# Optimization experiments

Measured on AMD Instinct MI355X. Metric: run time of the kernel, lower is better.

Reference implementation:

```python
import jax, jax.numpy as jnp
import numpy as np

B, S, H = 32, 4096, 512

def setup_inputs() -> dict:
    key = jax.random.key(0)
    k1, k2, k3 = jax.random.split(key, 3)
    h_t = jax.random.normal(k1, (B, H), dtype=jnp.float32)
    context = jax.random.normal(k2, (B, S, H), dtype=jnp.float32)
    W = jax.random.normal(k3, (H, H), dtype=jnp.float32) * (1.0 / np.sqrt(H))
    pos = 7  # current cyclic-buffer write index (self.it % seq_len)
    return {"h_t": h_t, "context": context, "W": W, "pos": pos}

def reference(h_t, context, W, pos):
    # Luong 'general' attention: score[b,s] = h_t[b] . (W @ context[b,s])
    scores = jnp.einsum('bh,hk,bsk->bs', h_t, W, context)  # [B,S]
    attn = jax.nn.softmax(scores, axis=-1)                  # softmax over buffer slots
    # weighted sum over the context buffer -> [B,H]
    cntx = jnp.einsum('bs,bsh->bh', attn, context)
    # cyclic buffer write: add_vector(h_t) at slot pos (detached in original)
    new_buffer = context.at[:, pos % context.shape[1], :].set(h_t)
    return cntx, new_buffer
```

## Files before the change

kernel.cpp:

```cpp
#include <hip/hip_runtime.h>
#include <math.h>

constexpr int B = 32, S = 4096, H = 512;
constexpr int BDIM = 256;
constexpr int MAX_SPLIT = 64;
constexpr float LOG2E = 1.44269504088896340736f;
constexpr float DEFER_THR = 11.5415603f;

typedef float f4 __attribute__((ext_vector_type(4)));

__global__ __launch_bounds__(BDIM) void u_kernel(const float* __restrict__ h_t,
                                                 const float* __restrict__ W,
                                                 float* __restrict__ u) {
    const int b = blockIdx.y;
    const int k = blockIdx.x * BDIM + threadIdx.x;
    __shared__ float hs[H];
    for (int i = threadIdx.x; i < H; i += BDIM) hs[i] = h_t[b * H + i];
    __syncthreads();
    float a0 = 0.f, a1 = 0.f, a2 = 0.f, a3 = 0.f;
#pragma unroll 8
    for (int h = 0; h < H; h += 4) {
        a0 = fmaf(hs[h],     W[(size_t)(h)     * H + k], a0);
        a1 = fmaf(hs[h + 1], W[(size_t)(h + 1) * H + k], a1);
        a2 = fmaf(hs[h + 2], W[(size_t)(h + 2) * H + k], a2);
        a3 = fmaf(hs[h + 3], W[(size_t)(h + 3) * H + k], a3);
    }
    u[b * H + k] = ((a0 + a1) + (a2 + a3)) * LOG2E;
}

__global__ __launch_bounds__(BDIM) void flash_kernel(const float* __restrict__ ctx,
                                                     const float* __restrict__ h_t,
                                                     const float* __restrict__ u,
                                                     const int* __restrict__ posp,
                                                     float* __restrict__ newbuf,
                                                     float* __restrict__ pacc,
                                                     float* __restrict__ pml,
                                                     int nsplit) {
    const int b     = blockIdx.y;
    const int split = blockIdx.x;
    const int w     = threadIdx.x >> 6;
    const int lane  = threadIdx.x & 63;
    const int rpb   = S / nsplit;
    const int s0    = split * rpb;
    int pos = posp[0] % S; if (pos < 0) pos += S;

    const f4* ub = (const f4*)(u + (size_t)b * H);
    const f4 u0 = ub[lane], u1 = ub[64 + lane];
    const f4* hb = (const f4*)(h_t + (size_t)b * H);
    const f4 h0 = hb[lane], h1 = hb[64 + lane];

    float m = -INFINITY, l = 0.f;
    f4 a0 = {0.f, 0.f, 0.f, 0.f}, a1 = {0.f, 0.f, 0.f, 0.f};

#pragma unroll 4
    for (int s = s0 + w; s < s0 + rpb; s += 4) {
        const f4* crow = (const f4*)(ctx + ((size_t)b * S + s) * H);
        const f4 c0 = crow[lane];
        const f4 c1 = crow[64 + lane];

        f4* orow = (f4*)(newbuf + ((size_t)b * S + s) * H);
        const f4 o0 = (s == pos) ? h0 : c0;
        const f4 o1 = (s == pos) ? h1 : c1;
        __builtin_nontemporal_store(o0, orow + lane);
        __builtin_nontemporal_store(o1, orow + 64 + lane);

        float d = c0.x * u0.x + c0.y * u0.y + c0.z * u0.z + c0.w * u0.w
                + c1.x * u1.x + c1.y * u1.y + c1.z * u1.z + c1.w * u1.w;
#pragma unroll
        for (int off = 32; off >= 1; off >>= 1) d += __shfl_xor(d, off);

        if (d > m + DEFER_THR) {
            const float sc = exp2f(m - d);
            a0 *= sc; a1 *= sc; l *= sc; m = d;
        }
        const float p = exp2f(d - m);
        a0 += p * c0;
        a1 += p * c1;
        l  += p;
    }

    __shared__ float lacc[4][H];
    __shared__ float lml[4][2];
    f4* dst = (f4*)&lacc[w][0];
    dst[lane] = a0; dst[64 + lane] = a1;
    if (lane == 0) { lml[w][0] = m; lml[w][1] = l; }
    __syncthreads();

    const float m0 = lml[0][0], m1 = lml[1][0], m2 = lml[2][0], m3 = lml[3][0];
    const float M  = fmaxf(fmaxf(m0, m1), fmaxf(m2, m3));
    const float e0 = exp2f(m0 - M), e1 = exp2f(m1 - M);
    const float e2 = exp2f(m2 - M), e3 = exp2f(m3 - M);

    const int t    = threadIdx.x;
    const int pidx = b * nsplit + split;
    const float ca = e0 * lacc[0][t]       + e1 * lacc[1][t]
                   + e2 * lacc[2][t]       + e3 * lacc[3][t];
    const float cb = e0 * lacc[0][256 + t] + e1 * lacc[1][256 + t]
                   + e2 * lacc[2][256 + t] + e3 * lacc[3][256 + t];
    pacc[(size_t)pidx * H + t]       = ca;
    pacc[(size_t)pidx * H + 256 + t] = cb;
    if (t == 0) {
        const float L = e0 * lml[0][1] + e1 * lml[1][1]
                      + e2 * lml[2][1] + e3 * lml[3][1];
        pml[2 * pidx] = M; pml[2 * pidx + 1] = L;
    }
}

__global__ __launch_bounds__(BDIM) void combine_kernel(const float* __restrict__ pacc,
                                                       const float* __restrict__ pml,
                                                       float* __restrict__ cntx,
                                                       int nsplit) {
    const int b    = blockIdx.x;
    const int half = blockIdx.y;
    const int t    = threadIdx.x;
    const int col  = half * 256 + t;

    __shared__ float lm[MAX_SPLIT], ll[MAX_SPLIT];
    for (int p = t; p < nsplit; p += BDIM) {
        lm[p] = pml[2 * (b * nsplit + p)];
        ll[p] = pml[2 * (b * nsplit + p) + 1];
    }
    __syncthreads();

    float M = -INFINITY;
    for (int p = 0; p < nsplit; ++p) M = fmaxf(M, lm[p]);

    float acc = 0.f, L = 0.f;
#pragma unroll 4
    for (int p = 0; p < nsplit; ++p) {
        const float e = exp2f(lm[p] - M);
        L   = fmaf(e, ll[p], L);
        acc = fmaf(e, pacc[(size_t)(b * nsplit + p) * H + col], acc);
    }
    cntx[b * H + col] = acc / L;
}

extern "C" void kernel_launch(void* const* d_in, const int* in_sizes, int n_in,
                              void* d_out, int out_size, void* d_ws, size_t ws_size,
                              hipStream_t stream) {
    const float* h_t = (const float*)d_in[0];
    const float* ctx = (const float*)d_in[1];
    const float* W   = (const float*)d_in[2];
    const int*   pos = (const int*)d_in[3];

    float* out    = (float*)d_out;
    float* cntx   = out;
    float* newbuf = out + (size_t)B * H;

    char*  ws = (char*)d_ws;
    float* u  = (float*)ws;
    const size_t u_bytes = (size_t)B * H * sizeof(float);

    int nsplit = MAX_SPLIT;
    while (nsplit > 1) {
        const size_t need = u_bytes
                          + (size_t)B * nsplit * H * sizeof(float)
                          + (size_t)B * nsplit * 2 * sizeof(float);
        if (need <= ws_size) break;
        nsplit >>= 1;
    }
    float* pacc = (float*)(ws + u_bytes);
    float* pml  = pacc + (size_t)B * nsplit * H;

    u_kernel<<<dim3(H / BDIM, B), BDIM, 0, stream>>>(h_t, W, u);
    flash_kernel<<<dim3(nsplit, B), BDIM, 0, stream>>>(ctx, h_t, u, pos, newbuf,
                                                       pacc, pml, nsplit);
    combine_kernel<<<dim3(B, 2), BDIM, 0, stream>>>(pacc, pml, cntx, nsplit);
}
```

Baseline: 122.6 us.

## Software-pipeline context loads with two independent softmax streams per warp

Measured after the change: 119.0 us, median of 2. 1.03x faster.

```diff
diff --git a/kernel.cpp b/kernel.cpp
--- a/kernel.cpp
+++ b/kernel.cpp
@@ -8,6 +8,15 @@
 constexpr float DEFER_THR = 11.5415603f;
 
 typedef float f4 __attribute__((ext_vector_type(4)));
+
+__device__ __forceinline__ float dot8(const f4 c0, const f4 c1,
+                                      const f4 u0, const f4 u1) {
+    float d = c0.x * u0.x;
+    d = fmaf(c0.y, u0.y, d); d = fmaf(c0.z, u0.z, d); d = fmaf(c0.w, u0.w, d);
+    d = fmaf(c1.x, u1.x, d); d = fmaf(c1.y, u1.y, d);
+    d = fmaf(c1.z, u1.z, d); d = fmaf(c1.w, u1.w, d);
+    return d;
+}
 
 __global__ __launch_bounds__(BDIM) void u_kernel(const float* __restrict__ h_t,
                                                  const float* __restrict__ W,
@@ -29,9 +38,7 @@
 }
 
 __global__ __launch_bounds__(BDIM) void flash_kernel(const float* __restrict__ ctx,
-                                                     const float* __restrict__ h_t,
                                                      const float* __restrict__ u,
-                                                     const int* __restrict__ posp,
                                                      float* __restrict__ newbuf,
                                                      float* __restrict__ pacc,
                                                      float* __restrict__ pml,
@@ -42,78 +49,114 @@
     const int lane  = threadIdx.x & 63;
     const int rpb   = S / nsplit;
     const int s0    = split * rpb;
-    int pos = posp[0] % S; if (pos < 0) pos += S;
+    const int halfr = rpb >> 1;
 
     const f4* ub = (const f4*)(u + (size_t)b * H);
     const f4 u0 = ub[lane], u1 = ub[64 + lane];
-    const f4* hb = (const f4*)(h_t + (size_t)b * H);
-    const f4 h0 = hb[lane], h1 = hb[64 + lane];
-
-    float m = -INFINITY, l = 0.f;
-    f4 a0 = {0.f, 0.f, 0.f, 0.f}, a1 = {0.f, 0.f, 0.f, 0.f};
-
-#pragma unroll 4
-    for (int s = s0 + w; s < s0 + rpb; s += 4) {
-        const f4* crow = (const f4*)(ctx + ((size_t)b * S + s) * H);
-        const f4 c0 = crow[lane];
-        const f4 c1 = crow[64 + lane];
-
-        f4* orow = (f4*)(newbuf + ((size_t)b * S + s) * H);
-        const f4 o0 = (s == pos) ? h0 : c0;
-        const f4 o1 = (s == pos) ? h1 : c1;
-        __builtin_nontemporal_store(o0, orow + lane);
-        __builtin_nontemporal_store(o1, orow + 64 + lane);
-
-        float d = c0.x * u0.x + c0.y * u0.y + c0.z * u0.z + c0.w * u0.w
-                + c1.x * u1.x + c1.y * u1.y + c1.z * u1.z + c1.w * u1.w;
-#pragma unroll
-        for (int off = 32; off >= 1; off >>= 1) d += __shfl_xor(d, off);
-
-        if (d > m + DEFER_THR) {
-            const float sc = exp2f(m - d);
-            a0 *= sc; a1 *= sc; l *= sc; m = d;
+
+    const size_t baseA = (size_t)b * S + s0;
+    const size_t baseB = baseA + halfr;
+
+    float mA = -INFINITY, lA = 0.f; f4 aA0 = {0,0,0,0}, aA1 = {0,0,0,0};
+    float mB = -INFINITY, lB = 0.f; f4 aB0 = {0,0,0,0}, aB1 = {0,0,0,0};
+
+    int r = w;
+    const f4* pA = (const f4*)(ctx + (baseA + r) * H);
+    const f4* pB = (const f4*)(ctx + (baseB + r) * H);
+    f4 cA0 = pA[lane], cA1 = pA[64 + lane];
+    f4 cB0 = pB[lane], cB1 = pB[64 + lane];
+
+    while (r < halfr) {
+        const int rn = r + 4;
+        const int rs = (rn < halfr) ? rn : r;
+        const f4* nA = (const f4*)(ctx + (baseA + rs) * H);
+        const f4* nB = (const f4*)(ctx + (baseB + rs) * H);
+        const f4 nA0 = nA[lane], nA1 = nA[64 + lane];
+        const f4 nB0 = nB[lane], nB1 = nB[64 + lane];
+
+        f4* oA = (f4*)(newbuf + (baseA + r) * H);
+        f4* oB = (f4*)(newbuf + (baseB + r) * H);
+        __builtin_nontemporal_store(cA0, oA + lane);
+        __builtin_nontemporal_store(cA1, oA + 64 + lane);
+        __builtin_nontemporal_store(cB0, oB + lane);
+        __builtin_nontemporal_store(cB1, oB + 64 + lane);
+
+        float dA = dot8(cA0, cA1, u0, u1);
+        float dB = dot8(cB0, cB1, u0, u1);
+#pragma unroll
+        for (int off = 32; off >= 1; off >>= 1) {
+            dA += __shfl_xor(dA, off);
+            dB += __shfl_xor(dB, off);
         }
-        const float p = exp2f(d - m);
-        a0 += p * c0;
-        a1 += p * c1;
-        l  += p;
-    }
-
-    __shared__ float lacc[4][H];
-    __shared__ float lml[4][2];
-    f4* dst = (f4*)&lacc[w][0];
-    dst[lane] = a0; dst[64 + lane] = a1;
-    if (lane == 0) { lml[w][0] = m; lml[w][1] = l; }
+
+        if (dA > mA + DEFER_THR) {
+            const float sc = exp2f(mA - dA);
+            aA0 *= sc; aA1 *= sc; lA *= sc; mA = dA;
+        }
+        if (dB > mB + DEFER_THR) {
+            const float sc = exp2f(mB - dB);
+            aB0 *= sc; aB1 *= sc; lB *= sc; mB = dB;
+        }
+        const float pAe = exp2f(dA - mA);
+        const float pBe = exp2f(dB - mB);
+        aA0 += pAe * cA0; aA1 += pAe * cA1; lA += pAe;
+        aB0 += pBe * cB0; aB1 += pBe * cB1; lB += pBe;
+
+        cA0 = nA0; cA1 = nA1; cB0 = nB0; cB1 = nB1;
+        r = rn;
+    }
+
+    __shared__ float lacc[8][H];
+    __shared__ float lml[8][2];
+    f4* dA_ = (f4*)&lacc[w][0];
+    f4* dB_ = (f4*)&lacc[4 + w][0];
+    dA_[lane] = aA0; dA_[64 + lane] = aA1;
+    dB_[lane] = aB0; dB_[64 + lane] = aB1;
+    if (lane == 0) {
+        lml[w][0] = mA;     lml[w][1] = lA;
+        lml[4 + w][0] = mB; lml[4 + w][1] = lB;
+    }
     __syncthreads();
 
-    const float m0 = lml[0][0], m1 = lml[1][0], m2 = lml[2][0], m3 = lml[3][0];
-    const float M  = fmaxf(fmaxf(m0, m1), fmaxf(m2, m3));
-    const float e0 = exp2f(m0 - M), e1 = exp2f(m1 - M);
-    const float e2 = exp2f(m2 - M), e3 = exp2f(m3 - M);
+    float M = -INFINITY;
+#pragma unroll
+    for (int j = 0; j < 8; ++j) M = fmaxf(M, lml[j][0]);
+    float e[8];
+#pragma unroll
+    for (int j = 0; j < 8; ++j) e[j] = exp2f(lml[j][0] - M);
 
     const int t    = threadIdx.x;
     const int pidx = b * nsplit + split;
-    const float ca = e0 * lacc[0][t]       + e1 * lacc[1][t]
-                   + e2 * lacc[2][t]       + e3 * lacc[3][t];
-    const float cb = e0 * lacc[0][256 + t] + e1 * lacc[1][256 + t]
-                   + e2 * lacc[2][256 + t] + e3 * lacc[3][256 + t];
+    float ca = 0.f, cb = 0.f;
+#pragma unroll
+    for (int j = 0; j < 8; ++j) {
+        ca = fmaf(e[j], lacc[j][t], ca);
+        cb = fmaf(e[j], lacc[j][256 + t], cb);
+    }
     pacc[(size_t)pidx * H + t]       = ca;
     pacc[(size_t)pidx * H + 256 + t] = cb;
     if (t == 0) {
-        const float L = e0 * lml[0][1] + e1 * lml[1][1]
-                      + e2 * lml[2][1] + e3 * lml[3][1];
+        float L = 0.f;
+#pragma unroll
+        for (int j = 0; j < 8; ++j) L = fmaf(e[j], lml[j][1], L);
         pml[2 * pidx] = M; pml[2 * pidx + 1] = L;
     }
 }
 
 __global__ __launch_bounds__(BDIM) void combine_kernel(const float* __restrict__ pacc,
                                                        const float* __restrict__ pml,
+                                                       const float* __restrict__ h_t,
+                                                       const int* __restrict__ posp,
+                                                       float* __restrict__ newbuf,
                                                        float* __restrict__ cntx,
                                                        int nsplit) {
     const int b    = blockIdx.x;
     const int half = blockIdx.y;
     const int t    = threadIdx.x;
     const int col  = half * 256 + t;
+
+    int pos = posp[0] % S; if (pos < 0) pos += S;
+    newbuf[((size_t)b * S + pos) * H + col] = h_t[b * H + col];
 
     __shared__ float lm[MAX_SPLIT], ll[MAX_SPLIT];
     for (int p = t; p < nsplit; p += BDIM) {
@@ -163,7 +206,8 @@
     float* pml  = pacc + (size_t)B * nsplit * H;
 
     u_kernel<<<dim3(H / BDIM, B), BDIM, 0, stream>>>(h_t, W, u);
-    flash_kernel<<<dim3(nsplit, B), BDIM, 0, stream>>>(ctx, h_t, u, pos, newbuf,
+    flash_kernel<<<dim3(nsplit, B), BDIM, 0, stream>>>(ctx, u, newbuf,
                                                        pacc, pml, nsplit);
-    combine_kernel<<<dim3(B, 2), BDIM, 0, stream>>>(pacc, pml, cntx, nsplit);
-}
+    combine_kernel<<<dim3(B, 2), BDIM, 0, stream>>>(pacc, pml, h_t, pos,
+                                                    newbuf, cntx, nsplit);
+}
```

## Process two rows per wavefront, split rows contiguously, move pos write to combine

Applied to the files above, without the earlier changes.

Result: no change. 122.2 us (-0.3%).

```diff
diff --git a/kernel.cpp b/kernel.cpp
--- a/kernel.cpp
+++ b/kernel.cpp
@@ -3,7 +3,7 @@
 
 constexpr int B = 32, S = 4096, H = 512;
 constexpr int BDIM = 256;
-constexpr int MAX_SPLIT = 64;
+constexpr int MAX_SPLIT = 128;
 constexpr float LOG2E = 1.44269504088896340736f;
 constexpr float DEFER_THR = 11.5415603f;
 
@@ -29,9 +29,7 @@
 }
 
 __global__ __launch_bounds__(BDIM) void flash_kernel(const float* __restrict__ ctx,
-                                                     const float* __restrict__ h_t,
                                                      const float* __restrict__ u,
-                                                     const int* __restrict__ posp,
                                                      float* __restrict__ newbuf,
                                                      float* __restrict__ pacc,
                                                      float* __restrict__ pml,
@@ -40,56 +38,86 @@
     const int split = blockIdx.x;
     const int w     = threadIdx.x >> 6;
     const int lane  = threadIdx.x & 63;
+    const int g     = lane >> 5;
+    const int j     = lane & 31;
     const int rpb   = S / nsplit;
-    const int s0    = split * rpb;
-    int pos = posp[0] % S; if (pos < 0) pos += S;
+    const int rpw   = rpb / 4;
+    const int s0    = split * rpb + w * rpw;
 
     const f4* ub = (const f4*)(u + (size_t)b * H);
-    const f4 u0 = ub[lane], u1 = ub[64 + lane];
-    const f4* hb = (const f4*)(h_t + (size_t)b * H);
-    const f4 h0 = hb[lane], h1 = hb[64 + lane];
+    f4 uf[4];
+#pragma unroll
+    for (int k = 0; k < 4; ++k) uf[k] = ub[j + 32 * k];
 
     float m = -INFINITY, l = 0.f;
-    f4 a0 = {0.f, 0.f, 0.f, 0.f}, a1 = {0.f, 0.f, 0.f, 0.f};
-
-#pragma unroll 4
-    for (int s = s0 + w; s < s0 + rpb; s += 4) {
-        const f4* crow = (const f4*)(ctx + ((size_t)b * S + s) * H);
-        const f4 c0 = crow[lane];
-        const f4 c1 = crow[64 + lane];
-
-        f4* orow = (f4*)(newbuf + ((size_t)b * S + s) * H);
-        const f4 o0 = (s == pos) ? h0 : c0;
-        const f4 o1 = (s == pos) ? h1 : c1;
-        __builtin_nontemporal_store(o0, orow + lane);
-        __builtin_nontemporal_store(o1, orow + 64 + lane);
-
-        float d = c0.x * u0.x + c0.y * u0.y + c0.z * u0.z + c0.w * u0.w
-                + c1.x * u1.x + c1.y * u1.y + c1.z * u1.z + c1.w * u1.w;
-#pragma unroll
-        for (int off = 32; off >= 1; off >>= 1) d += __shfl_xor(d, off);
+    f4 acc[4] = {{0,0,0,0},{0,0,0,0},{0,0,0,0},{0,0,0,0}};
+
+#pragma unroll 2
+    for (int r = 0; r < rpw; r += 2) {
+        const size_t row = (size_t)b * S + s0 + r + g;
+        const f4* crow = (const f4*)(ctx + row * H);
+        f4 c[4];
+#pragma unroll
+        for (int k = 0; k < 4; ++k) c[k] = crow[j + 32 * k];
+
+        f4* orow = (f4*)(newbuf + row * H);
+#pragma unroll
+        for (int k = 0; k < 4; ++k)
+            __builtin_nontemporal_store(c[k], orow + j + 32 * k);
+
+        float d = c[0].x * uf[0].x;
+        d = fmaf(c[0].y, uf[0].y, d); d = fmaf(c[0].z, uf[0].z, d);
+        d = fmaf(c[0].w, uf[0].w, d);
+#pragma unroll
+        for (int k = 1; k < 4; ++k) {
+            d = fmaf(c[k].x, uf[k].x, d); d = fmaf(c[k].y, uf[k].y, d);
+            d = fmaf(c[k].z, uf[k].z, d); d = fmaf(c[k].w, uf[k].w, d);
+        }
+#pragma unroll
+        for (int off = 16; off >= 1; off >>= 1) d += __shfl_xor(d, off);
 
         if (d > m + DEFER_THR) {
             const float sc = exp2f(m - d);
-            a0 *= sc; a1 *= sc; l *= sc; m = d;
+#pragma unroll
+            for (int k = 0; k < 4; ++k) acc[k] *= sc;
+            l *= sc; m = d;
         }
         const float p = exp2f(d - m);
-        a0 += p * c0;
-        a1 += p * c1;
-        l  += p;
+#pragma unroll
+        for (int k = 0; k < 4; ++k) acc[k] += p * c[k];
+        l += p;
+    }
+
+    const float mo = __shfl_xor(m, 32);
+    const float lo = __shfl_xor(l, 32);
+    const float M  = fmaxf(m, mo);
+    const float es = exp2f(m - M), eo = exp2f(mo - M);
+    const float lw = es * l + eo * lo;
+    f4 am[4];
+#pragma unroll
+    for (int k = 0; k < 4; ++k) {
+        f4 other;
+        other.x = __shfl_xor(acc[k].x, 32);
+        other.y = __shfl_xor(acc[k].y, 32);
+        other.z = __shfl_xor(acc[k].z, 32);
+        other.w = __shfl_xor(acc[k].w, 32);
+        am[k] = es * acc[k] + eo * other;
     }
 
     __shared__ float lacc[4][H];
     __shared__ float lml[4][2];
-    f4* dst = (f4*)&lacc[w][0];
-    dst[lane] = a0; dst[64 + lane] = a1;
-    if (lane == 0) { lml[w][0] = m; lml[w][1] = l; }
+    if (g == 0) {
+        f4* dst = (f4*)&lacc[w][0];
+#pragma unroll
+        for (int k = 0; k < 4; ++k) dst[j + 32 * k] = am[k];
+        if (j == 0) { lml[w][0] = M; lml[w][1] = lw; }
+    }
     __syncthreads();
 
     const float m0 = lml[0][0], m1 = lml[1][0], m2 = lml[2][0], m3 = lml[3][0];
-    const float M  = fmaxf(fmaxf(m0, m1), fmaxf(m2, m3));
-    const float e0 = exp2f(m0 - M), e1 = exp2f(m1 - M);
-    const float e2 = exp2f(m2 - M), e3 = exp2f(m3 - M);
+    const float Mb = fmaxf(fmaxf(m0, m1), fmaxf(m2, m3));
+    const float e0 = exp2f(m0 - Mb), e1 = exp2f(m1 - Mb);
+    const float e2 = exp2f(m2 - Mb), e3 = exp2f(m3 - Mb);
 
     const int t    = threadIdx.x;
     const int pidx = b * nsplit + split;
@@ -102,18 +130,24 @@
     if (t == 0) {
         const float L = e0 * lml[0][1] + e1 * lml[1][1]
                       + e2 * lml[2][1] + e3 * lml[3][1];
-        pml[2 * pidx] = M; pml[2 * pidx + 1] = L;
+        pml[2 * pidx] = Mb; pml[2 * pidx + 1] = L;
     }
 }
 
 __global__ __launch_bounds__(BDIM) void combine_kernel(const float* __restrict__ pacc,
                                                        const float* __restrict__ pml,
+                                                       const float* __restrict__ h_t,
+                                                       const int* __restrict__ posp,
+                                                       float* __restrict__ newbuf,
                                                        float* __restrict__ cntx,
                                                        int nsplit) {
     const int b    = blockIdx.x;
     const int half = blockIdx.y;
     const int t    = threadIdx.x;
     const int col  = half * 256 + t;
+
+    int pos = posp[0] % S; if (pos < 0) pos += S;
+    newbuf[((size_t)b * S + pos) * H + col] = h_t[b * H + col];
 
     __shared__ float lm[MAX_SPLIT], ll[MAX_SPLIT];
     for (int p = t; p < nsplit; p += BDIM) {
@@ -163,7 +197,8 @@
     float* pml  = pacc + (size_t)B * nsplit * H;
 
     u_kernel<<<dim3(H / BDIM, B), BDIM, 0, stream>>>(h_t, W, u);
-    flash_kernel<<<dim3(nsplit, B), BDIM, 0, stream>>>(ctx, h_t, u, pos, newbuf,
+    flash_kernel<<<dim3(nsplit, B), BDIM, 0, stream>>>(ctx, u, newbuf,
                                                        pacc, pml, nsplit);
-    combine_kernel<<<dim3(B, 2), BDIM, 0, stream>>>(pacc, pml, cntx, nsplit);
-}
+    combine_kernel<<<dim3(B, 2), BDIM, 0, stream>>>(pacc, pml, h_t, pos,
+                                                    newbuf, cntx, nsplit);
+}
```
